# Kernel optimization log

Measured on AMD Instinct MI355X. Metric: run time of the kernel, lower is better.

Reference implementation:

```python
import jax, jax.numpy as jnp
import numpy as np
from functools import partial

POOL_LIST = (1, 2, 4)   # SPP pyramid: 1 + 4 + 16 = 21 bins per channel
NUM_ROIS = 256
H = 64
W = 64
C = 512


def setup_inputs() -> dict:
    key = jax.random.key(0)
    k1, k2, k3 = jax.random.split(key, 3)
    img = jax.random.normal(k1, (1, H, W, C), dtype=jnp.float32)
    # rois = (x, y, w, h) in feature-map pixels; chosen so every bin is
    # non-empty and in-bounds (x+h <= W, y+w <= H given the code's axis swap).
    xy = jax.random.uniform(k2, (1, NUM_ROIS, 2), jnp.float32, 0.0, 32.0)
    wh = jax.random.uniform(k3, (1, NUM_ROIS, 2), jnp.float32, 8.0, 31.0)
    rois = jnp.concatenate([xy, wh], axis=-1)
    return {"img": img, "rois": rois}


@partial(jax.jit, static_argnames=("pool_list",))
def _roi_pool(img, rois, pool_list):
    feat = img[0]                     # (H, W, C), channels_last
    Hf, Wf, Cc = feat.shape
    R = rois.shape[1]
    x = rois[0, :, 0]
    y = rois[0, :, 1]
    w = rois[0, :, 2]
    h = rois[0, :, 3]
    wi = jnp.arange(Wf)
    hi = jnp.arange(Hf)
    NEG = jnp.asarray(-jnp.inf, feat.dtype)
    outs = []
    for p in pool_list:               # small static pyramid loop
        # Faithful to original: x-axis bin length uses h/p (col_length),
        # y-axis bin length uses w/p (row_length).
        col_len = h / p               # (R,) for x direction
        row_len = w / p               # (R,) for y direction
        idx = jnp.arange(p, dtype=rois.dtype)
        # bin boundaries, round-half-to-even like tf.round / K.round
        x1 = jnp.round(x[:, None] + idx * col_len[:, None]).astype(jnp.int32)        # (R, p)
        x2 = jnp.round(x[:, None] + (idx + 1.0) * col_len[:, None]).astype(jnp.int32)
        y1 = jnp.round(y[:, None] + idx * row_len[:, None]).astype(jnp.int32)
        y2 = jnp.round(y[:, None] + (idx + 1.0) * row_len[:, None]).astype(jnp.int32)
        mx = (wi >= x1[..., None]) & (wi < x2[..., None])   # (R, p, W)
        my = (hi >= y1[..., None]) & (hi < y2[..., None])   # (R, p, H)
        # masked max over W per (roi, x-bin): fused select+reduce under jit
        colmax = jnp.max(jnp.where(mx[:, :, None, :, None], feat[None, None], NEG), axis=3)  # (R, p, H, C)
        # masked max over H per (roi, x-bin, y-bin)
        binmax = jnp.max(jnp.where(my[:, None, :, :, None], colmax[:, :, None, :, :], NEG), axis=3)  # (R, p_ix, p_jy, C)
        # original loop order: ix outer, jy inner, channels fastest
        outs.append(binmax.reshape(R, p * p, Cc))
    out = jnp.concatenate(outs, axis=1)   # (R, sum(p*p), C)
    return out.reshape(1, R, -1)          # (1, num_rois, C * 21)


def reference(img, rois):
    return _roi_pool(img, rois, POOL_LIST)
```

## Files before the change

kernel.cpp:

```cpp
#include <hip/hip_runtime.h>
#include <math.h>

#define HF 64
#define WF 64
#define CC 512
#define NROI 256
#define NBINS 21


__global__ __launch_bounds__(64) void roi_pool_fine(
    const float* __restrict__ img,
    const float* __restrict__ rois,
    float* __restrict__ out)
{
    const int bid = blockIdx.x;
    const int x7  = bid & 7;
    const int q   = x7 >> 1;
    const int wu  = ((bid >> 3) << 1) | (bid & 1);
    const int roi = wu >> 4;
    const int bin = wu & 15;
    const int jx  = bin >> 2;
    const int jy  = bin & 3;
    const int c0  = q * 128 + threadIdx.x * 2;

    const float x = rois[roi * 4 + 0];
    const float y = rois[roi * 4 + 1];
    const float w = rois[roi * 4 + 2];
    const float h = rois[roi * 4 + 3];

    const float clh = h * 0.25f;
    const float clw = w * 0.25f;

    const int x1 = (int)rintf(__fadd_rn(x, __fmul_rn((float)jx,       clh)));
    const int x2 = (int)rintf(__fadd_rn(x, __fmul_rn((float)(jx + 1), clh)));
    const int y1 = (int)rintf(__fadd_rn(y, __fmul_rn((float)jy,       clw)));
    const int y2 = (int)rintf(__fadd_rn(y, __fmul_rn((float)(jy + 1), clw)));

    float2 acc;
    acc.x = -INFINITY;
    acc.y = -INFINITY;

    const float* base = img + c0;
    for (int hh = y1; hh < y2; ++hh) {
        const float* rowp = base + (size_t)hh * (WF * CC);
        for (int ww = x1; ww < x2; ++ww) {
            const float2 v = *(const float2*)(rowp + (size_t)ww * CC);
            acc.x = fmaxf(acc.x, v.x);
            acc.y = fmaxf(acc.y, v.y);
        }
    }

    float* outr = out + (size_t)roi * (NBINS * CC) + c0;
    *(float2*)(outr + (size_t)(5 + jx * 4 + jy) * CC) = acc;
}

__global__ __launch_bounds__(64) void roi_pool_coarse(
    float* __restrict__ out)
{
    const int bid = blockIdx.x;
    const int x7  = bid & 7;
    const int q   = x7 >> 1;
    const int roi = ((bid >> 3) << 1) | (bid & 1);
    const int c0  = q * 128 + threadIdx.x * 2;

    float* outr = out + (size_t)roi * (NBINS * CC) + c0;

    float2 fine[4][4];
#pragma unroll
    for (int ix = 0; ix < 4; ++ix)
#pragma unroll
        for (int iy = 0; iy < 4; ++iy)
            fine[ix][iy] = *(const float2*)(outr + (size_t)(5 + ix * 4 + iy) * CC);

    float2 qv[2][2];
#pragma unroll
    for (int i2 = 0; i2 < 2; ++i2)
#pragma unroll
        for (int j2 = 0; j2 < 2; ++j2) {
            float2 v;
            v.x = fmaxf(fmaxf(fine[2*i2][2*j2].x, fine[2*i2+1][2*j2].x),
                        fmaxf(fine[2*i2][2*j2+1].x, fine[2*i2+1][2*j2+1].x));
            v.y = fmaxf(fmaxf(fine[2*i2][2*j2].y, fine[2*i2+1][2*j2].y),
                        fmaxf(fine[2*i2][2*j2+1].y, fine[2*i2+1][2*j2+1].y));
            qv[i2][j2] = v;
            *(float2*)(outr + (size_t)(1 + i2 * 2 + j2) * CC) = v;
        }

    float2 g;
    g.x = fmaxf(fmaxf(qv[0][0].x, qv[0][1].x), fmaxf(qv[1][0].x, qv[1][1].x));
    g.y = fmaxf(fmaxf(qv[0][0].y, qv[0][1].y), fmaxf(qv[1][0].y, qv[1][1].y));
    *(float2*)(outr) = g;
}

extern "C" void kernel_launch(void* const* d_in, const int* in_sizes, int n_in,
                              void* d_out, int out_size, void* d_ws, size_t ws_size,
                              hipStream_t stream) {
    const float* img  = (const float*)d_in[0];
    const float* rois = (const float*)d_in[1];
    float* out = (float*)d_out;

    dim3 gridA(NROI * 16 * 4);
    dim3 blockA(64);
    roi_pool_fine<<<gridA, blockA, 0, stream>>>(img, rois, out);

    dim3 gridB(NROI * 4);
    roi_pool_coarse<<<gridB, blockA, 0, stream>>>(out);
}
```

Measured before the change: 25.42 us.

## Widen fine ROI kernel to float4 loads with split-column shuffle reduction

The fine-bin kernel now uses 256-thread blocks that hold the four x-bins of one (roi, y-bin, channel quarter). Each wavefront splits the bin's columns between two half-waves that read float4 channel vectors, and the halves are merged with a cross-lane shuffle. The coarse kernel also moves to float4 and splits the work across half-waves. This cuts the block count and the instruction count per byte, but adds a divergent branch in the column loop, and half the lanes sit idle during the stores.

```diff
diff --git a/kernel.cpp b/kernel.cpp
--- a/kernel.cpp
+++ b/kernel.cpp
@@ -7,21 +7,30 @@
 #define NROI 256
 #define NBINS 21
 
+__device__ __forceinline__ float4 max4(float4 a, float4 b) {
+    float4 r;
+    r.x = fmaxf(a.x, b.x); r.y = fmaxf(a.y, b.y);
+    r.z = fmaxf(a.z, b.z); r.w = fmaxf(a.w, b.w);
+    return r;
+}
 
-__global__ __launch_bounds__(64) void roi_pool_fine(
+__global__ __launch_bounds__(256) void roi_pool_fine(
     const float* __restrict__ img,
     const float* __restrict__ rois,
     float* __restrict__ out)
 {
-    const int bid = blockIdx.x;
-    const int x7  = bid & 7;
-    const int q   = x7 >> 1;
-    const int wu  = ((bid >> 3) << 1) | (bid & 1);
-    const int roi = wu >> 4;
-    const int bin = wu & 15;
-    const int jx  = bin >> 2;
-    const int jy  = bin & 3;
-    const int c0  = q * 128 + threadIdx.x * 2;
+    const int bid  = blockIdx.x;
+    const int x7   = bid & 7;
+    const int q    = x7 >> 1;
+    const int rest = ((bid >> 3) << 1) | (bid & 1);
+    const int roi  = rest >> 2;
+    const int jy   = rest & 3;
+    const int tid  = threadIdx.x;
+    const int jx   = tid >> 6;
+    const int lane = tid & 63;
+    const int half = lane >> 5;
+    const int cl   = lane & 31;
+    const int c0   = q * 128 + cl * 4;
 
     const float x = rois[roi * 4 + 0];
     const float y = rois[roi * 4 + 1];
@@ -36,60 +45,69 @@
     const int y1 = (int)rintf(__fadd_rn(y, __fmul_rn((float)jy,       clw)));
     const int y2 = (int)rintf(__fadd_rn(y, __fmul_rn((float)(jy + 1), clw)));
 
-    float2 acc;
-    acc.x = -INFINITY;
-    acc.y = -INFINITY;
+    float4 acc;
+    acc.x = -INFINITY; acc.y = -INFINITY; acc.z = -INFINITY; acc.w = -INFINITY;
 
     const float* base = img + c0;
     for (int hh = y1; hh < y2; ++hh) {
         const float* rowp = base + (size_t)hh * (WF * CC);
-        for (int ww = x1; ww < x2; ++ww) {
-            const float2 v = *(const float2*)(rowp + (size_t)ww * CC);
-            acc.x = fmaxf(acc.x, v.x);
-            acc.y = fmaxf(acc.y, v.y);
+        for (int ww0 = x1; ww0 < x2; ww0 += 2) {
+            const int ww = ww0 + half;
+            if (ww < x2) {
+                const float4 v = *(const float4*)(rowp + (size_t)ww * CC);
+                acc = max4(acc, v);
+            }
         }
     }
 
-    float* outr = out + (size_t)roi * (NBINS * CC) + c0;
-    *(float2*)(outr + (size_t)(5 + jx * 4 + jy) * CC) = acc;
+    acc.x = fmaxf(acc.x, __shfl_xor(acc.x, 32));
+    acc.y = fmaxf(acc.y, __shfl_xor(acc.y, 32));
+    acc.z = fmaxf(acc.z, __shfl_xor(acc.z, 32));
+    acc.w = fmaxf(acc.w, __shfl_xor(acc.w, 32));
+
+    if (half == 0) {
+        float* outr = out + (size_t)roi * (NBINS * CC) + c0;
+        *(float4*)(outr + (size_t)(5 + jx * 4 + jy) * CC) = acc;
+    }
 }
 
 __global__ __launch_bounds__(64) void roi_pool_coarse(
     float* __restrict__ out)
 {
-    const int bid = blockIdx.x;
-    const int x7  = bid & 7;
-    const int q   = x7 >> 1;
-    const int roi = ((bid >> 3) << 1) | (bid & 1);
-    const int c0  = q * 128 + threadIdx.x * 2;
+    const int bid  = blockIdx.x;
+    const int q    = (bid & 7) >> 1;
+    const int roi  = ((bid >> 3) << 1) | (bid & 1);
+    const int lane = threadIdx.x;
+    const int h2   = lane >> 5;
+    const int cl   = lane & 31;
+    const int c0   = q * 128 + cl * 4;
 
     float* outr = out + (size_t)roi * (NBINS * CC) + c0;
 
-    float2 fine[4][4];
+    float4 f[2][4];
 #pragma unroll
-    for (int ix = 0; ix < 4; ++ix)
+    for (int a = 0; a < 2; ++a)
 #pragma unroll
         for (int iy = 0; iy < 4; ++iy)
-            fine[ix][iy] = *(const float2*)(outr + (size_t)(5 + ix * 4 + iy) * CC);
+            f[a][iy] = *(const float4*)(outr + (size_t)(5 + (2 * h2 + a) * 4 + iy) * CC);
 
-    float2 qv[2][2];
+    float4 p2v[2];
 #pragma unroll
-    for (int i2 = 0; i2 < 2; ++i2)
-#pragma unroll
-        for (int j2 = 0; j2 < 2; ++j2) {
-            float2 v;
-            v.x = fmaxf(fmaxf(fine[2*i2][2*j2].x, fine[2*i2+1][2*j2].x),
-                        fmaxf(fine[2*i2][2*j2+1].x, fine[2*i2+1][2*j2+1].x));
-            v.y = fmaxf(fmaxf(fine[2*i2][2*j2].y, fine[2*i2+1][2*j2].y),
-                        fmaxf(fine[2*i2][2*j2+1].y, fine[2*i2+1][2*j2+1].y));
-            qv[i2][j2] = v;
-            *(float2*)(outr + (size_t)(1 + i2 * 2 + j2) * CC) = v;
-        }
+    for (int j2 = 0; j2 < 2; ++j2) {
+        float4 v = max4(max4(f[0][2 * j2], f[0][2 * j2 + 1]),
+                        max4(f[1][2 * j2], f[1][2 * j2 + 1]));
+        *(float4*)(outr + (size_t)(1 + h2 * 2 + j2) * CC) = v;
+        p2v[j2] = v;
+    }
 
-    float2 g;
-    g.x = fmaxf(fmaxf(qv[0][0].x, qv[0][1].x), fmaxf(qv[1][0].x, qv[1][1].x));
-    g.y = fmaxf(fmaxf(qv[0][0].y, qv[0][1].y), fmaxf(qv[1][0].y, qv[1][1].y));
-    *(float2*)(outr) = g;
+    float4 m = max4(p2v[0], p2v[1]);
+    m.x = fmaxf(m.x, __shfl_xor(m.x, 32));
+    m.y = fmaxf(m.y, __shfl_xor(m.y, 32));
+    m.z = fmaxf(m.z, __shfl_xor(m.z, 32));
+    m.w = fmaxf(m.w, __shfl_xor(m.w, 32));
+    if (h2 == 0) {
+        *(float4*)(outr) = m;
+    }
 }
 
 extern "C" void kernel_launch(void* const* d_in, const int* in_sizes, int n_in,
@@ -99,10 +117,11 @@
     const float* rois = (const float*)d_in[1];
     float* out = (float*)d_out;
 
-    dim3 gridA(NROI * 16 * 4);
-    dim3 blockA(64);
+    dim3 gridA(NROI * 4 * 4);
+    dim3 blockA(256);
     roi_pool_fine<<<gridA, blockA, 0, stream>>>(img, rois, out);
 
     dim3 gridB(NROI * 4);
-    roi_pool_coarse<<<gridB, blockA, 0, stream>>>(out);
+    dim3 blockB(64);
+    roi_pool_coarse<<<gridB, blockB, 0, stream>>>(out);
 }
```

Measured after the change: 22.29 us. 1.14x faster.
